# Kernel optimization log

Measured on AMD Instinct MI355X. Metric: run time of the kernel, lower is better.

## Reference

```python
import jax, jax.numpy as jnp
import numpy as np

N, E = 50000, 500000
IN, C, CE_IN = 128, 64, 16   # raw node dim, mid_channel, raw edge dim
L = 3                        # num_layers: layer0 = bare conv, layers 1..2 = res+ blocks
LN_EPS = 1e-5


def layer_norm(x, g, b):
    mu = x.mean(-1, keepdims=True)
    var = ((x - mu) ** 2).mean(-1, keepdims=True)
    return (x - mu) * jax.lax.rsqrt(var + LN_EPS) * g + b


def sage_conv(x, e, src, dst, W1, b1, W2, b2, Wr, t):
    """SAGEConvV2 with softmax aggregation. Returns (node_out, per-edge messages)."""
    # message: lin_l(cat([x_i, x_j, edge_attr])) ; x_i = dst (target), x_j = src (source)
    m_in = jnp.concatenate([x[dst], x[src], e], axis=-1)          # [E, 2C+Ce]
    m = jax.nn.relu(m_in @ W1 + b1) @ W2 + b2                      # [E, C]
    # scatter_softmax(m * t, dst) per feature channel
    logits = m * t
    seg_max = jax.ops.segment_max(logits, dst, num_segments=N)    # [N, C]
    w = jnp.exp(logits - seg_max[dst])
    w = w / jax.ops.segment_sum(w, dst, num_segments=N)[dst]
    out = jax.ops.segment_sum(m * w, dst, num_segments=N)         # [N, C]
    out = out + x @ Wr                                             # root weight (no bias)
    return out, m


def setup_inputs() -> dict:
    key = jax.random.key(0)
    ks = jax.random.split(key, 18)
    f32 = jnp.float32

    def w(k, shape, fan_in):
        return (jax.random.normal(k, shape, f32) / np.sqrt(fan_in)).astype(f32)

    inp = {
        "x": jax.random.normal(ks[0], (N, IN), f32),
        "edge_index": jax.random.randint(ks[1], (2, E), 0, N, dtype=jnp.int64),
        "edge_attr": jax.random.normal(ks[2], (E, CE_IN), f32),
        # encoders
        "node_W": w(ks[3], (IN, C), IN),
        "node_b": jnp.zeros((C,), f32),
        "edge_W": w(ks[4], (CE_IN, C), CE_IN),
        "edge_b": jnp.zeros((C,), f32),
        # stacked conv params (L convs, identical shapes)
        "conv_W1": w(ks[5], (L, 3 * C, 2 * C), 3 * C),
        "conv_b1": jnp.zeros((L, 2 * C), f32),
        "conv_W2": w(ks[6], (L, 2 * C, C), 2 * C),
        "conv_b2": jnp.zeros((L, C), f32),
        "conv_Wr": w(ks[7], (L, C, C), C),
        "conv_t": jnp.ones((L,), f32),
        # layer norms: ln_g[0]/ln_b[0] used as the final output norm, 1..2 inside res+ blocks
        "ln_g": jnp.ones((L, C), f32),
        "ln_b": jnp.zeros((L, C), f32),
        "eln_g": jnp.ones((L - 1, C), f32),
        "eln_b": jnp.zeros((L - 1, C), f32),
    }
    return inp


def reference(x, edge_index, edge_attr, node_W, node_b, edge_W, edge_b,
              conv_W1, conv_b1, conv_W2, conv_b2, conv_Wr, conv_t,
              ln_g, ln_b, eln_g, eln_b):
    src, dst = edge_index[0], edge_index[1]
    h = x @ node_W + node_b                    # node encoder
    e = edge_attr @ edge_W + edge_b            # edge encoder
    # first layer: bare conv
    h, e = sage_conv(h, e, src, dst, conv_W1[0], conv_b1[0], conv_W2[0],
                     conv_b2[0], conv_Wr[0], conv_t[0])
    # res+ blocks (dropout is identity in eval mode)
    for i in range(1, L):
        hn = jax.nn.relu(layer_norm(h, ln_g[i], ln_b[i]))
        en = layer_norm(e, eln_g[i - 1], eln_b[i - 1])
        dh, m = sage_conv(hn, en, src, dst, conv_W1[i], conv_b1[i], conv_W2[i],
                          conv_b2[i], conv_Wr[i], conv_t[i])
        h = h + dh
        e = e + m
    # final norm + act (uses layer-0 norm params, as in the canonical DeeperGCN example)
    return jax.nn.relu(layer_norm(h, ln_g[0], ln_b[0]))
```

## Files before the change

### kernel.cpp

```cpp
#include <hip/hip_runtime.h>

typedef unsigned short u16;
typedef unsigned int u32;
typedef __attribute__((ext_vector_type(8))) short short8;
typedef __attribute__((ext_vector_type(4))) float floatx4;

#define LN_EPS 1e-5f

__device__ __forceinline__ float bf2f(u16 u) {
    union { u32 i; float f; } v; v.i = ((u32)u) << 16; return v.f;
}
__device__ __forceinline__ u16 f2bf(float f) {
    union { u32 i; float f; } v; v.f = f;
    u32 x = v.i;
    return (u16)((x + 0x7fffu + ((x >> 16) & 1u)) >> 16);
}
__device__ __forceinline__ int clampi(int v, int lo, int hi) {
    return v < lo ? lo : (v > hi ? hi : v);
}

__global__ void k_fill(float* __restrict__ out, int nel, float val) {
    int i = blockIdx.x * blockDim.x + threadIdx.x;
    if (i < nel) out[i] = val;
}

__global__ void k_zero(int* p, int n) {
    int i = blockIdx.x * blockDim.x + threadIdx.x;
    if (i < n) p[i] = 0;
}

__global__ void k_detect(const int* __restrict__ ei, int E, int* __restrict__ flag) {
    __shared__ int any;
    if (threadIdx.x == 0) any = 0;
    __syncthreads();
    int lim = (E < 4096) ? E : 4096;
    int v = 0;
    for (int i = threadIdx.x; i < lim; i += 256) v |= ei[2 * i + 1];
    if (v) atomicOr(&any, 1);
    __syncthreads();
    if (threadIdx.x == 0) flag[0] = (any == 0) ? 1 : 0;
}

__global__ void k_hist(const int* __restrict__ ei, const int* __restrict__ flag,
                       int* __restrict__ deg, int E, int n) {
    int e = blockIdx.x * blockDim.x + threadIdx.x;
    if (e < E) {
        int d = flag[0] ? ei[2 * ((size_t)E + e)] : ei[(size_t)E + e];
        atomicAdd(&deg[clampi(d, 0, n - 1)], 1);
    }
}

__global__ void k_scan1(const int* __restrict__ deg, int* __restrict__ offs,
                        int* __restrict__ bsum, int n) {
    __shared__ int s[256];
    int t = threadIdx.x;
    int i = blockIdx.x * 256 + t;
    int v = (i < n) ? deg[i] : 0;
    s[t] = v; __syncthreads();
    for (int off = 1; off < 256; off <<= 1) {
        int x = (t >= off) ? s[t - off] : 0;
        __syncthreads();
        s[t] += x;
        __syncthreads();
    }
    if (i < n) offs[i] = s[t] - v;
    if (t == 255) bsum[blockIdx.x] = s[255];
}

__global__ void k_scan2(int* bsum, int nb) {
    __shared__ int s[256];
    int t = threadIdx.x;
    int v = (t < nb) ? bsum[t] : 0;
    s[t] = v; __syncthreads();
    for (int off = 1; off < 256; off <<= 1) {
        int x = (t >= off) ? s[t - off] : 0;
        __syncthreads();
        s[t] += x;
        __syncthreads();
    }
    if (t < nb) bsum[t] = s[t] - v;
}

__global__ void k_scan3(int* __restrict__ offs, const int* __restrict__ bsum,
                        int* __restrict__ cursor, int n, int E) {
    int i = blockIdx.x * 256 + threadIdx.x;
    if (i < n) {
        int v = offs[i] + bsum[blockIdx.x];
        offs[i] = v;
        cursor[i] = v;
    }
    if (i == 0) offs[n] = E;
}

__global__ void k_scatter(const int* __restrict__ ei, const int* __restrict__ flag,
                          int* __restrict__ cursor,
                          int* __restrict__ perm, int* __restrict__ srcs,
                          int* __restrict__ dsts, int E, int n) {
    int e = blockIdx.x * blockDim.x + threadIdx.x;
    if (e < E) {
        int sv, dv;
        if (flag[0]) {
            sv = ei[2 * (size_t)e];
            dv = ei[2 * ((size_t)E + e)];
        } else {
            sv = ei[e];
            dv = ei[(size_t)E + e];
        }
        sv = clampi(sv, 0, n - 1);
        dv = clampi(dv, 0, n - 1);
        int p = clampi(atomicAdd(&cursor[dv], 1), 0, E - 1);
        perm[p] = e;
        srcs[p] = sv;
        dsts[p] = dv;
    }
}

__global__ void k_swz(const float* __restrict__ W1, const float* __restrict__ W2,
                      const float* __restrict__ Wr, const float* __restrict__ nW,
                      u16* __restrict__ W1s, u16* __restrict__ W2s,
                      u16* __restrict__ Wrs, u16* __restrict__ nWs) {
    int i = blockIdx.x * blockDim.x + threadIdx.x;
    if (i < 3 * 24576) {
        int l = i / 24576, rem = i % 24576;
        int k = rem / 128, n = rem % 128;
        int kt = k >> 5, q = (k >> 3) & 3, j = k & 7;
        W1s[l * 24576 + ((kt * 4 + q) * 128 + n) * 8 + j] = f2bf(W1[i]);
    }
    if (i < 3 * 8192) {
        int l = i / 8192, rem = i % 8192;
        int k = rem / 64, n = rem % 64;
        int kt = k >> 5, q = (k >> 3) & 3, j = k & 7;
        W2s[l * 8192 + ((kt * 4 + q) * 64 + n) * 8 + j] = f2bf(W2[i]);
    }
    if (i < 3 * 4096) {
        int l = i / 4096, rem = i % 4096;
        int k = rem / 64, n = rem % 64;
        int kt = k >> 5, q = (k >> 3) & 3, j = k & 7;
        Wrs[l * 4096 + ((kt * 4 + q) * 64 + n) * 8 + j] = f2bf(Wr[i]);
    }
    if (i < 8192) {
        int k = i / 64, n = i % 64;
        int kt = k >> 5, q = (k >> 3) & 3, j = k & 7;
        nWs[((kt * 4 + q) * 64 + n) * 8 + j] = f2bf(nW[i]);
    }
}

__global__ __launch_bounds__(512) void k_node_enc(
    const float* __restrict__ x, const u16* __restrict__ nWs, const float* __restrict__ bias,
    float* __restrict__ h, u16* __restrict__ hn, int n) {
    int t = threadIdx.x;
    int w = t >> 6, l = t & 63, q = l >> 4, ml = l & 15;
    int wbase = blockIdx.x * 128 + w * 16;
    int rin = wbase + ml;
    int rr = (rin < n) ? rin : 0;
    const float* xr = x + (size_t)rr * 128;
    short8 a[4];
#pragma unroll
    for (int kt = 0; kt < 4; kt++) {
        float4 f0 = *((const float4*)(xr + kt * 32 + q * 8));
        float4 f1 = *((const float4*)(xr + kt * 32 + q * 8 + 4));
        a[kt][0] = (short)f2bf(f0.x); a[kt][1] = (short)f2bf(f0.y);
        a[kt][2] = (short)f2bf(f0.z); a[kt][3] = (short)f2bf(f0.w);
        a[kt][4] = (short)f2bf(f1.x); a[kt][5] = (short)f2bf(f1.y);
        a[kt][6] = (short)f2bf(f1.z); a[kt][7] = (short)f2bf(f1.w);
    }
    float bc[4];
#pragma unroll
    for (int nt = 0; nt < 4; nt++) bc[nt] = bias[nt * 16 + ml];
    floatx4 acc[4];
#pragma unroll
    for (int nt = 0; nt < 4; nt++) acc[nt] = floatx4{0.f, 0.f, 0.f, 0.f};
#pragma unroll
    for (int kt = 0; kt < 4; kt++) {
#pragma unroll
        for (int nt = 0; nt < 4; nt++) {
            short8 bf = *((const short8*)(nWs + (size_t)((kt * 4 + q) * 64 + nt * 16 + ml) * 8));
            acc[nt] = __builtin_amdgcn_mfma_f32_16x16x32_bf16(a[kt], bf, acc[nt], 0, 0, 0);
        }
    }
#pragma unroll
    for (int nt = 0; nt < 4; nt++) {
#pragma unroll
        for (int r2 = 0; r2 < 4; r2++) {
            int pos = wbase + q * 4 + r2;
            if (pos < n) {
                float v = acc[nt][r2] + bc[nt];
                size_t idx = (size_t)pos * 64 + nt * 16 + ml;
                h[idx] = v;
                hn[idx] = f2bf(v);
            }
        }
    }
}

__global__ __launch_bounds__(256) void k_edge_enc(
    const float* __restrict__ ea, const int* __restrict__ perm,
    const float* __restrict__ W, const float* __restrict__ bias,
    u16* __restrict__ e_s, int E) {
    __shared__ float4 sW4[16 * 16];
    int t = threadIdx.x;
    if (t < 256) sW4[t] = ((const float4*)W)[t];
    __syncthreads();
    int gid = blockIdx.x * 256 + t;
    int eidx = gid >> 2, qq = gid & 3;
    if (eidx >= E) return;
    int e = perm[eidx];
    const float4* row4 = (const float4*)(ea + (size_t)e * 16);
    float4 r4[4];
    r4[0] = row4[0]; r4[1] = row4[1]; r4[2] = row4[2]; r4[3] = row4[3];
    const float* row = (const float*)r4;
    float4 acc[4];
#pragma unroll
    for (int j = 0; j < 4; j++) acc[j] = ((const float4*)bias)[qq * 4 + j];
#pragma unroll
    for (int k = 0; k < 16; k++) {
        float rv = row[k];
#pragma unroll
        for (int j = 0; j < 4; j++) {
            float4 wv = sW4[k * 16 + qq * 4 + j];
            acc[j].x += rv * wv.x; acc[j].y += rv * wv.y;
            acc[j].z += rv * wv.z; acc[j].w += rv * wv.w;
        }
    }
    u32 pk[8];
#pragma unroll
    for (int j = 0; j < 4; j++) {
        pk[2 * j]     = (u32)f2bf(acc[j].x) | ((u32)f2bf(acc[j].y) << 16);
        pk[2 * j + 1] = (u32)f2bf(acc[j].z) | ((u32)f2bf(acc[j].w) << 16);
    }
    uint4* outp = (uint4*)(e_s + (size_t)eidx * 64 + qq * 16);
    outp[0] = make_uint4(pk[0], pk[1], pk[2], pk[3]);
    outp[1] = make_uint4(pk[4], pk[5], pk[6], pk[7]);
}

#define TILE 256
#define HSTR 136
__global__ __launch_bounds__(512, 4) void k_mlp(
    const u16* __restrict__ hn, const u16* __restrict__ e_s,
    const u16* __restrict__ e_s2,
    const int* __restrict__ dsts, const int* __restrict__ srcs,
    const u16* __restrict__ W1s, const float* __restrict__ b1,
    const u16* __restrict__ W2s, const float* __restrict__ b2,
    const float* __restrict__ elng, const float* __restrict__ elnb,
    int ln_edge, u16* __restrict__ m_out, int E) {
    __shared__ __align__(16) short sW2L[8192];
    __shared__ __align__(16) short sShared[24576];

    int t = threadIdx.x;
    int w = t >> 6, l = t & 63, q = l >> 4, ml = l & 15;
    int base = blockIdx.x * TILE + w * 32;
    int pos0 = base + ml;
    int pos1 = base + 16 + ml;
    bool act0 = pos0 < E, act1 = pos1 < E;
    int pp0 = act0 ? pos0 : 0, pp1 = act1 ? pos1 : 0;
    int dn0 = act0 ? dsts[pos0] : 0;
    int sn0 = act0 ? srcs[pos0] : 0;
    int dn1 = act1 ? dsts[pos1] : 0;
    int sn1 = act1 ? srcs[pos1] : 0;

    short8 a0[6], a1[6];
    a0[0] = *(const short8*)(hn + (size_t)dn0 * 64 + q * 8);
    a0[1] = *(const short8*)(hn + (size_t)dn0 * 64 + 32 + q * 8);
    a0[2] = *(const short8*)(hn + (size_t)sn0 * 64 + q * 8);
    a0[3] = *(const short8*)(hn + (size_t)sn0 * 64 + 32 + q * 8);
    a1[0] = *(const short8*)(hn + (size_t)dn1 * 64 + q * 8);
    a1[1] = *(const short8*)(hn + (size_t)dn1 * 64 + 32 + q * 8);
    a1[2] = *(const short8*)(hn + (size_t)sn1 * 64 + q * 8);
    a1[3] = *(const short8*)(hn + (size_t)sn1 * 64 + 32 + q * 8);
    short8 e00 = *(const short8*)(e_s + (size_t)pp0 * 64 + q * 8);
    short8 e01 = *(const short8*)(e_s + (size_t)pp0 * 64 + 32 + q * 8);
    short8 e10 = *(const short8*)(e_s + (size_t)pp1 * 64 + q * 8);
    short8 e11 = *(const short8*)(e_s + (size_t)pp1 * 64 + 32 + q * 8);
    short8 f00, f01, f10, f11;
    bool has2 = (e_s2 != nullptr);
    if (has2) {
        f00 = *(const short8*)(e_s2 + (size_t)pp0 * 64 + q * 8);
        f01 = *(const short8*)(e_s2 + (size_t)pp0 * 64 + 32 + q * 8);
        f10 = *(const short8*)(e_s2 + (size_t)pp1 * 64 + q * 8);
        f11 = *(const short8*)(e_s2 + (size_t)pp1 * 64 + 32 + q * 8);
    }

    {
        const uint4* g1 = (const uint4*)W1s;
        uint4* s1 = (uint4*)sShared;
#pragma unroll
        for (int j = 0; j < 6; j++) s1[t + j * 512] = g1[t + j * 512];
        const uint4* g2 = (const uint4*)W2s;
        uint4* s2 = (uint4*)sW2L;
#pragma unroll
        for (int j = 0; j < 2; j++) s2[t + j * 512] = g2[t + j * 512];
    }

    if (ln_edge) {
        {
            float ev[16];
            float sm = 0.f, sq = 0.f;
#pragma unroll
            for (int i = 0; i < 8; i++) {
                float f0 = bf2f((u16)e00[i]);
                float f1 = bf2f((u16)e01[i]);
                if (has2) { f0 += bf2f((u16)f00[i]); f1 += bf2f((u16)f01[i]); }
                ev[i] = f0; ev[8 + i] = f1;
                sm += f0 + f1; sq += f0 * f0 + f1 * f1;
            }
            sm += __shfl_xor(sm, 16); sm += __shfl_xor(sm, 32);
            sq += __shfl_xor(sq, 16); sq += __shfl_xor(sq, 32);
            float mu = sm * (1.f / 64.f);
            float var = sq * (1.f / 64.f) - mu * mu;
            float inv = rsqrtf(fmaxf(var, 0.f) + LN_EPS);
#pragma unroll
            for (int i = 0; i < 8; i++) {
                int c0 = q * 8 + i, c1 = 32 + q * 8 + i;
                a0[4][i] = (short)f2bf((ev[i] - mu) * inv * elng[c0] + elnb[c0]);
                a0[5][i] = (short)f2bf((ev[8 + i] - mu) * inv * elng[c1] + elnb[c1]);
            }
        }
        {
            float ev[16];
            float sm = 0.f, sq = 0.f;
#pragma unroll
            for (int i = 0; i < 8; i++) {
                float f0 = bf2f((u16)e10[i]);
                float f1 = bf2f((u16)e11[i]);
                if (has2) { f0 += bf2f((u16)f10[i]); f1 += bf2f((u16)f11[i]); }
                ev[i] = f0; ev[8 + i] = f1;
                sm += f0 + f1; sq += f0 * f0 + f1 * f1;
            }
            sm += __shfl_xor(sm, 16); sm += __shfl_xor(sm, 32);
            sq += __shfl_xor(sq, 16); sq += __shfl_xor(sq, 32);
            float mu = sm * (1.f / 64.f);
            float var = sq * (1.f / 64.f) - mu * mu;
            float inv = rsqrtf(fmaxf(var, 0.f) + LN_EPS);
#pragma unroll
            for (int i = 0; i < 8; i++) {
                int c0 = q * 8 + i, c1 = 32 + q * 8 + i;
                a1[4][i] = (short)f2bf((ev[i] - mu) * inv * elng[c0] + elnb[c0]);
                a1[5][i] = (short)f2bf((ev[8 + i] - mu) * inv * elng[c1] + elnb[c1]);
            }
        }
    } else {
        a0[4] = e00; a0[5] = e01;
        a1[4] = e10; a1[5] = e11;
    }

    __syncthreads();

    floatx4 acc0[8], acc1[8];
#pragma unroll
    for (int nt = 0; nt < 8; nt++) {
        acc0[nt] = floatx4{0.f, 0.f, 0.f, 0.f};
        acc1[nt] = floatx4{0.f, 0.f, 0.f, 0.f};
    }
#pragma unroll
    for (int kt = 0; kt < 6; kt++) {
#pragma unroll
        for (int nt = 0; nt < 8; nt++) {
            short8 bf = *((const short8*)(sShared + ((kt * 4 + q) * 128 + nt * 16 + ml) * 8));
            acc0[nt] = __builtin_amdgcn_mfma_f32_16x16x32_bf16(a0[kt], bf, acc0[nt], 0, 0, 0);
            acc1[nt] = __builtin_amdgcn_mfma_f32_16x16x32_bf16(a1[kt], bf, acc1[nt], 0, 0, 0);
        }
    }

    __syncthreads();

    float b1c[8], b2c[4];
#pragma unroll
    for (int nt = 0; nt < 8; nt++) b1c[nt] = b1[nt * 16 + ml];
#pragma unroll
    for (int nt = 0; nt < 4; nt++) b2c[nt] = b2[nt * 16 + ml];

    short* arena = sShared + w * 16 * HSTR;

#pragma unroll
    for (int nt = 0; nt < 8; nt++) {
#pragma unroll
        for (int r2 = 0; r2 < 4; r2++) {
            float v = fmaxf(acc0[nt][r2] + b1c[nt], 0.f);
            ((u16*)arena)[(q * 4 + r2) * HSTR + nt * 16 + ml] = f2bf(v);
        }
    }
    short8 ah0[4];
#pragma unroll
    for (int kt = 0; kt < 4; kt++)
        ah0[kt] = *((const short8*)(arena + ml * HSTR + kt * 32 + q * 8));

#pragma unroll
    for (int nt = 0; nt < 8; nt++) {
#pragma unroll
        for (int r2 = 0; r2 < 4; r2++) {
            float v = fmaxf(acc1[nt][r2] + b1c[nt], 0.f);
            ((u16*)arena)[(q * 4 + r2) * HSTR + nt * 16 + ml] = f2bf(v);
        }
    }
    short8 ah1[4];
#pragma unroll
    for (int kt = 0; kt < 4; kt++)
        ah1[kt] = *((const short8*)(arena + ml * HSTR + kt * 32 + q * 8));

    floatx4 c20[4], c21[4];
#pragma unroll
    for (int nt = 0; nt < 4; nt++) {
        c20[nt] = floatx4{0.f, 0.f, 0.f, 0.f};
        c21[nt] = floatx4{0.f, 0.f, 0.f, 0.f};
    }
#pragma unroll
    for (int kt = 0; kt < 4; kt++) {
#pragma unroll
        for (int nt = 0; nt < 4; nt++) {
            short8 bf = *((const short8*)(sW2L + ((kt * 4 + q) * 64 + nt * 16 + ml) * 8));
            c20[nt] = __builtin_amdgcn_mfma_f32_16x16x32_bf16(ah0[kt], bf, c20[nt], 0, 0, 0);
            c21[nt] = __builtin_amdgcn_mfma_f32_16x16x32_bf16(ah1[kt], bf, c21[nt], 0, 0, 0);
        }
    }

#pragma unroll
    for (int nt = 0; nt < 4; nt++) {
#pragma unroll
        for (int r2 = 0; r2 < 4; r2++) {
            ((u16*)arena)[(q * 4 + r2) * HSTR + nt * 16 + ml] = f2bf(c20[nt][r2] + b2c[nt]);
        }
    }
    {
        short8 m0 = *((const short8*)(arena + ml * HSTR + q * 16));
        short8 m1 = *((const short8*)(arena + ml * HSTR + q * 16 + 8));
        if (act0) {
            *((short8*)(m_out + (size_t)pos0 * 64 + q * 16)) = m0;
            *((short8*)(m_out + (size_t)pos0 * 64 + q * 16 + 8)) = m1;
        }
    }
#pragma unroll
    for (int nt = 0; nt < 4; nt++) {
#pragma unroll
        for (int r2 = 0; r2 < 4; r2++) {
            ((u16*)arena)[(q * 4 + r2) * HSTR + nt * 16 + ml] = f2bf(c21[nt][r2] + b2c[nt]);
        }
    }
    {
        short8 m0 = *((const short8*)(arena + ml * HSTR + q * 16));
        short8 m1 = *((const short8*)(arena + ml * HSTR + q * 16 + 8));
        if (act1) {
            *((short8*)(m_out + (size_t)pos1 * 64 + q * 16)) = m0;
            *((short8*)(m_out + (size_t)pos1 * 64 + q * 16 + 8)) = m1;
        }
    }
}

__global__ __launch_bounds__(512) void k_root(
    const u16* __restrict__ hn, const u16* __restrict__ Wrs,
    float* __restrict__ h, int add_h, int n) {
    __shared__ short sA[8 * 1024];
    int t = threadIdx.x;
    int base = blockIdx.x * 128;
    {
        int r = t >> 2, s = t & 3;
        int pos = base + r;
        int g = r >> 4, m = r & 15;
        short* grp = sA + g * 1024;
        bool act = pos < n;
        uint4 z4 = make_uint4(0, 0, 0, 0);
        const uint4* pd = (const uint4*)(hn + (size_t)(act ? pos : 0) * 64);
        uint4 d0 = act ? pd[2 * s] : z4;
        uint4 d1 = act ? pd[2 * s + 1] : z4;
        int ch = (s >> 1) * 4 + (s & 1) * 2;
        *((uint4*)(grp + ch * 128 + m * 8)) = d0;
        *((uint4*)(grp + (ch + 1) * 128 + m * 8)) = d1;
    }
    __syncthreads();
    int w = t >> 6, l = t & 63, q = l >> 4, ml = l & 15;
    short* arena = sA + w * 1024;
    floatx4 acc[4];
#pragma unroll
    for (int nt = 0; nt < 4; nt++) acc[nt] = floatx4{0.f, 0.f, 0.f, 0.f};
#pragma unroll
    for (int kt = 0; kt < 2; kt++) {
        short8 a = *((const short8*)(arena + (kt * 4 + q) * 128 + ml * 8));
#pragma unroll
        for (int nt = 0; nt < 4; nt++) {
            short8 bf = *((const short8*)(Wrs + (size_t)((kt * 4 + q) * 64 + nt * 16 + ml) * 8));
            acc[nt] = __builtin_amdgcn_mfma_f32_16x16x32_bf16(a, bf, acc[nt], 0, 0, 0);
        }
    }
#pragma unroll
    for (int nt = 0; nt < 4; nt++) {
#pragma unroll
        for (int r2 = 0; r2 < 4; r2++) {
            int pos = base + w * 16 + q * 4 + r2;
            if (pos < n) {
                size_t idx = (size_t)pos * 64 + nt * 16 + ml;
                float v = acc[nt][r2];
                h[idx] = add_h ? (h[idx] + v) : v;
            }
        }
    }
}

__global__ __launch_bounds__(256) void k_agg2(
    const u16* __restrict__ m_s, float* __restrict__ h,
    const int* __restrict__ offs, const float* __restrict__ tptr, int tidx,
    const float* __restrict__ g, const float* __restrict__ b,
    u16* __restrict__ hn_out, float* __restrict__ f32_out,
    int write_h, int n, int E) {
    int t = threadIdx.x, wid = t >> 6, lane = t & 63;
    float tv = tptr[tidx];
    float gc = g[lane], bc = b[lane];
    for (int node = blockIdx.x * 4 + wid; node < n; node += gridDim.x * 4) {
        int p0 = clampi(offs[node], 0, E);
        int p1 = clampi(offs[node + 1], p0, E);
        float M = -1e30f, D = 0.f, S = 0.f;
        int p = p0;
        for (; p + 1 < p1; p += 2) {
            float mv0 = bf2f(m_s[(size_t)p * 64 + lane]);
            float mv1 = bf2f(m_s[(size_t)(p + 1) * 64 + lane]);
            float lg0 = mv0 * tv, lg1 = mv1 * tv;
            float Mp = fmaxf(lg0, lg1);
            float a0 = __expf(lg0 - Mp), a1 = __expf(lg1 - Mp);
            float Dp = a0 + a1, Sp = mv0 * a0 + mv1 * a1;
            float Mn = fmaxf(M, Mp);
            float xx = __expf(M - Mn), yy = __expf(Mp - Mn);
            D = D * xx + Dp * yy;
            S = S * xx + Sp * yy;
            M = Mn;
        }
        if (p < p1) {
            float mv = bf2f(m_s[(size_t)p * 64 + lane]);
            float lg = mv * tv;
            float Mn = fmaxf(M, lg);
            float xx = __expf(M - Mn), yy = __expf(lg - Mn);
            D = D * xx + yy;
            S = S * xx + mv * yy;
        }
        float hv = h[(size_t)node * 64 + lane];
        if (p1 > p0) hv += S / D;
        if (write_h) h[(size_t)node * 64 + lane] = hv;
        float s = hv;
#pragma unroll
        for (int o = 32; o > 0; o >>= 1) s += __shfl_xor(s, o);
        float mu = s * (1.f / 64.f);
        float d = hv - mu;
        float s2 = d * d;
#pragma unroll
        for (int o = 32; o > 0; o >>= 1) s2 += __shfl_xor(s2, o);
        float inv = rsqrtf(s2 * (1.f / 64.f) + LN_EPS);
        float r = fmaxf(d * inv * gc + bc, 0.f);
        if (hn_out) hn_out[(size_t)node * 64 + lane] = f2bf(r);
        else        f32_out[(size_t)node * 64 + lane] = r;
    }
}

extern "C" void kernel_launch(void* const* d_in, const int* in_sizes, int n_in,
                              void* d_out, int out_size, void* d_ws, size_t ws_size,
                              hipStream_t stream) {
    float* outp = (float*)d_out;
    int FB = (out_size + 255) / 256;

    if (n_in != 17) {
        k_fill<<<FB, 256, 0, stream>>>(outp, out_size, 3.0f);
        return;
    }

    const float* x    = (const float*)d_in[0];
    const int*   ei   = (const int*)d_in[1];
    const float* ea   = (const float*)d_in[2];
    const float* nW   = (const float*)d_in[3];
    const float* nb   = (const float*)d_in[4];
    const float* eW   = (const float*)d_in[5];
    const float* eb   = (const float*)d_in[6];
    const float* cW1  = (const float*)d_in[7];
    const float* cb1  = (const float*)d_in[8];
    const float* cW2  = (const float*)d_in[9];
    const float* cb2  = (const float*)d_in[10];
    const float* cWr  = (const float*)d_in[11];
    const float* ct   = (const float*)d_in[12];
    const float* lng  = (const float*)d_in[13];
    const float* lnb  = (const float*)d_in[14];
    const float* elng = (const float*)d_in[15];
    const float* elnb = (const float*)d_in[16];

    const int n = in_sizes[0] / 128;
    const int E = in_sizes[2] / 16;

    char* ws = (char*)d_ws;
    size_t o = 0;
    auto alloc = [&](size_t bytes) -> void* {
        void* p = ws + o;
        o += (bytes + 255) & ~(size_t)255;
        return p;
    };
    int*   flag   = (int*)alloc(256);
    int*   deg    = (int*)alloc((size_t)n * 4);
    int*   offs   = (int*)alloc((size_t)(n + 1) * 4);
    int*   cursor = (int*)alloc((size_t)n * 4);
    int*   bsum   = (int*)alloc(256 * 4);
    int*   perm   = (int*)alloc((size_t)E * 4);
    int*   srcs   = (int*)alloc((size_t)E * 4);
    int*   dsts   = (int*)alloc((size_t)E * 4);
    float* h      = (float*)alloc((size_t)n * 64 * 4);
    u16*   hn     = (u16*)alloc((size_t)n * 64 * 2);
    u16*   bufA   = (u16*)alloc((size_t)E * 64 * 2);
    u16*   bufB   = (u16*)alloc((size_t)E * 64 * 2);
    u16*   W1s    = (u16*)alloc((size_t)3 * 24576 * 2);
    u16*   W2s    = (u16*)alloc((size_t)3 * 8192 * 2);
    u16*   Wrs    = (u16*)alloc((size_t)3 * 4096 * 2);
    u16*   nWs    = (u16*)alloc((size_t)8192 * 2);

    k_fill<<<FB, 256, 0, stream>>>(outp, out_size, 1.0f);
    if (o > ws_size) {
        k_fill<<<FB, 256, 0, stream>>>(outp, out_size, 2.0f);
        return;
    }

    int SB = (n + 255) / 256;
    k_detect<<<1, 256, 0, stream>>>(ei, E, flag);
    k_zero<<<SB, 256, 0, stream>>>(deg, n);
    k_hist<<<(E + 255) / 256, 256, 0, stream>>>(ei, flag, deg, E, n);
    k_scan1<<<SB, 256, 0, stream>>>(deg, offs, bsum, n);
    k_scan2<<<1, 256, 0, stream>>>(bsum, SB);
    k_scan3<<<SB, 256, 0, stream>>>(offs, bsum, cursor, n, E);
    k_scatter<<<(E + 255) / 256, 256, 0, stream>>>(ei, flag, cursor, perm, srcs, dsts, E, n);
    k_swz<<<(3 * 24576 + 255) / 256, 256, 0, stream>>>(cW1, cW2, cWr, nW, W1s, W2s, Wrs, nWs);
    k_node_enc<<<(n + 127) / 128, 512, 0, stream>>>(x, nWs, nb, h, hn, n);
    k_edge_enc<<<(E * 4 + 255) / 256, 256, 0, stream>>>(ea, perm, eW, eb, bufA, E);

    int MB = (E + TILE - 1) / TILE;
    int RB = (n + 127) / 128;
    int AB = (n + 3) / 4;

    const u16* mlp_in[3]  = { bufA, bufB, bufB };
    const u16* mlp_in2[3] = { nullptr, nullptr, bufA };
    u16*       mlp_out[3] = { bufB, bufA, bufA };

    for (int i = 0; i < 3; i++) {
        k_mlp<<<MB, 512, 0, stream>>>(
            hn, mlp_in[i], mlp_in2[i], dsts, srcs,
            W1s + (size_t)i * 24576, cb1 + (size_t)i * 128,
            W2s + (size_t)i * 8192, cb2 + (size_t)i * 64,
            elng + (size_t)((i > 0) ? (i - 1) : 0) * 64,
            elnb + (size_t)((i > 0) ? (i - 1) : 0) * 64,
            (i > 0) ? 1 : 0, mlp_out[i], E);
        k_root<<<RB, 512, 0, stream>>>(hn, Wrs + (size_t)i * 4096, h, (i > 0) ? 1 : 0, n);
        if (i < 2) {
            k_agg2<<<AB, 256, 0, stream>>>(mlp_out[i], h, offs, ct, i,
                                           lng + (size_t)(i + 1) * 64, lnb + (size_t)(i + 1) * 64,
                                           hn, nullptr, 1, n, E);
        } else {
            k_agg2<<<AB, 256, 0, stream>>>(mlp_out[i], h, offs, ct, i,
                                           lng, lnb,
                                           nullptr, outp, 0, n, E);
        }
    }
}
```

Measured before the change: 527.4 us.

## Fuse root-weight GEMM into node encoder and aggregation, drop k_root

Removes the standalone k_root launch by computing the layer-0 root term x@Wr inside the node encoder, and computing each next layer's root term inside k_agg2 right after LayerNorm. The shuffle-based dot product uses Wr staged in shared memory. It also merges the detect and zero kernels into one launch. This saves three launches and an extra read-modify-write of h per layer. In exchange, k_agg2 loads 8KB of weights into LDS per block and does 64 shuffle-FMAs per lane per node on scalar ALUs rather than MFMA, which may slow the aggregation kernel.

```diff
diff --git a/kernel.cpp b/kernel.cpp
--- a/kernel.cpp
+++ b/kernel.cpp
@@ -24,21 +24,22 @@
     if (i < nel) out[i] = val;
 }
 
-__global__ void k_zero(int* p, int n) {
-    int i = blockIdx.x * blockDim.x + threadIdx.x;
-    if (i < n) p[i] = 0;
-}
-
-__global__ void k_detect(const int* __restrict__ ei, int E, int* __restrict__ flag) {
-    __shared__ int any;
-    if (threadIdx.x == 0) any = 0;
-    __syncthreads();
-    int lim = (E < 4096) ? E : 4096;
-    int v = 0;
-    for (int i = threadIdx.x; i < lim; i += 256) v |= ei[2 * i + 1];
-    if (v) atomicOr(&any, 1);
-    __syncthreads();
-    if (threadIdx.x == 0) flag[0] = (any == 0) ? 1 : 0;
+__global__ void k_pre0(const int* __restrict__ ei, int E, int* __restrict__ flag,
+                       int* __restrict__ deg, int n) {
+    int t = threadIdx.x;
+    if (blockIdx.x == 0) {
+        __shared__ int any;
+        if (t == 0) any = 0;
+        __syncthreads();
+        int lim = (E < 4096) ? E : 4096;
+        int v = 0;
+        for (int i = t; i < lim; i += 256) v |= ei[2 * i + 1];
+        if (v) atomicOr(&any, 1);
+        __syncthreads();
+        if (t == 0) flag[0] = (any == 0) ? 1 : 0;
+    }
+    int i = blockIdx.x * 256 + t;
+    if (i < n) deg[i] = 0;
 }
 
 __global__ void k_hist(const int* __restrict__ ei, const int* __restrict__ flag,
@@ -118,7 +119,8 @@
 __global__ void k_swz(const float* __restrict__ W1, const float* __restrict__ W2,
                       const float* __restrict__ Wr, const float* __restrict__ nW,
                       u16* __restrict__ W1s, u16* __restrict__ W2s,
-                      u16* __restrict__ Wrs, u16* __restrict__ nWs) {
+                      u16* __restrict__ Wrs, u16* __restrict__ nWs,
+                      u16* __restrict__ WrKC) {
     int i = blockIdx.x * blockDim.x + threadIdx.x;
     if (i < 3 * 24576) {
         int l = i / 24576, rem = i % 24576;
@@ -137,6 +139,7 @@
         int k = rem / 64, n = rem % 64;
         int kt = k >> 5, q = (k >> 3) & 3, j = k & 7;
         Wrs[l * 4096 + ((kt * 4 + q) * 64 + n) * 8 + j] = f2bf(Wr[i]);
+        WrKC[i] = f2bf(Wr[i]);
     }
     if (i < 8192) {
         int k = i / 64, n = i % 64;
@@ -145,9 +148,13 @@
     }
 }
 
+#define HSTR 136
+
 __global__ __launch_bounds__(512) void k_node_enc(
     const float* __restrict__ x, const u16* __restrict__ nWs, const float* __restrict__ bias,
+    const u16* __restrict__ Wrs0,
     float* __restrict__ h, u16* __restrict__ hn, int n) {
+    __shared__ short sA[8 * 16 * HSTR];
     int t = threadIdx.x;
     int w = t >> 6, l = t & 63, q = l >> 4, ml = l & 15;
     int wbase = blockIdx.x * 128 + w * 16;
@@ -178,17 +185,39 @@
             acc[nt] = __builtin_amdgcn_mfma_f32_16x16x32_bf16(a[kt], bf, acc[nt], 0, 0, 0);
         }
     }
+    short* arena = sA + w * 16 * HSTR;
 #pragma unroll
     for (int nt = 0; nt < 4; nt++) {
 #pragma unroll
         for (int r2 = 0; r2 < 4; r2++) {
             int pos = wbase + q * 4 + r2;
-            if (pos < n) {
-                float v = acc[nt][r2] + bc[nt];
-                size_t idx = (size_t)pos * 64 + nt * 16 + ml;
-                h[idx] = v;
-                hn[idx] = f2bf(v);
-            }
+            float v = acc[nt][r2] + bc[nt];
+            u16 bv = f2bf(v);
+            arena[(q * 4 + r2) * HSTR + nt * 16 + ml] = (short)bv;
+            if (pos < n) hn[(size_t)pos * 64 + nt * 16 + ml] = bv;
+        }
+    }
+    short8 ah[2];
+#pragma unroll
+    for (int kt = 0; kt < 2; kt++)
+        ah[kt] = *((const short8*)(arena + ml * HSTR + kt * 32 + q * 8));
+    floatx4 acc2[4];
+#pragma unroll
+    for (int nt = 0; nt < 4; nt++) acc2[nt] = floatx4{0.f, 0.f, 0.f, 0.f};
+#pragma unroll
+    for (int kt = 0; kt < 2; kt++) {
+#pragma unroll
+        for (int nt = 0; nt < 4; nt++) {
+            short8 bf = *((const short8*)(Wrs0 + (size_t)((kt * 4 + q) * 64 + nt * 16 + ml) * 8));
+            acc2[nt] = __builtin_amdgcn_mfma_f32_16x16x32_bf16(ah[kt], bf, acc2[nt], 0, 0, 0);
+        }
+    }
+#pragma unroll
+    for (int nt = 0; nt < 4; nt++) {
+#pragma unroll
+        for (int r2 = 0; r2 < 4; r2++) {
+            int pos = wbase + q * 4 + r2;
+            if (pos < n) h[(size_t)pos * 64 + nt * 16 + ml] = acc2[nt][r2];
         }
     }
 }
@@ -234,7 +263,6 @@
 }
 
 #define TILE 256
-#define HSTR 136
 __global__ __launch_bounds__(512, 4) void k_mlp(
     const u16* __restrict__ hn, const u16* __restrict__ e_s,
     const u16* __restrict__ e_s2,
@@ -445,62 +473,20 @@
     }
 }
 
-__global__ __launch_bounds__(512) void k_root(
-    const u16* __restrict__ hn, const u16* __restrict__ Wrs,
-    float* __restrict__ h, int add_h, int n) {
-    __shared__ short sA[8 * 1024];
-    int t = threadIdx.x;
-    int base = blockIdx.x * 128;
-    {
-        int r = t >> 2, s = t & 3;
-        int pos = base + r;
-        int g = r >> 4, m = r & 15;
-        short* grp = sA + g * 1024;
-        bool act = pos < n;
-        uint4 z4 = make_uint4(0, 0, 0, 0);
-        const uint4* pd = (const uint4*)(hn + (size_t)(act ? pos : 0) * 64);
-        uint4 d0 = act ? pd[2 * s] : z4;
-        uint4 d1 = act ? pd[2 * s + 1] : z4;
-        int ch = (s >> 1) * 4 + (s & 1) * 2;
-        *((uint4*)(grp + ch * 128 + m * 8)) = d0;
-        *((uint4*)(grp + (ch + 1) * 128 + m * 8)) = d1;
-    }
-    __syncthreads();
-    int w = t >> 6, l = t & 63, q = l >> 4, ml = l & 15;
-    short* arena = sA + w * 1024;
-    floatx4 acc[4];
-#pragma unroll
-    for (int nt = 0; nt < 4; nt++) acc[nt] = floatx4{0.f, 0.f, 0.f, 0.f};
-#pragma unroll
-    for (int kt = 0; kt < 2; kt++) {
-        short8 a = *((const short8*)(arena + (kt * 4 + q) * 128 + ml * 8));
-#pragma unroll
-        for (int nt = 0; nt < 4; nt++) {
-            short8 bf = *((const short8*)(Wrs + (size_t)((kt * 4 + q) * 64 + nt * 16 + ml) * 8));
-            acc[nt] = __builtin_amdgcn_mfma_f32_16x16x32_bf16(a, bf, acc[nt], 0, 0, 0);
-        }
-    }
-#pragma unroll
-    for (int nt = 0; nt < 4; nt++) {
-#pragma unroll
-        for (int r2 = 0; r2 < 4; r2++) {
-            int pos = base + w * 16 + q * 4 + r2;
-            if (pos < n) {
-                size_t idx = (size_t)pos * 64 + nt * 16 + ml;
-                float v = acc[nt][r2];
-                h[idx] = add_h ? (h[idx] + v) : v;
-            }
-        }
-    }
-}
-
 __global__ __launch_bounds__(256) void k_agg2(
     const u16* __restrict__ m_s, float* __restrict__ h,
     const int* __restrict__ offs, const float* __restrict__ tptr, int tidx,
     const float* __restrict__ g, const float* __restrict__ b,
+    const u16* __restrict__ wrkc,
     u16* __restrict__ hn_out, float* __restrict__ f32_out,
-    int write_h, int n, int E) {
+    int n, int E) {
+    __shared__ u16 sWr[4096];
     int t = threadIdx.x, wid = t >> 6, lane = t & 63;
+    bool haveW = (wrkc != nullptr);
+    if (haveW) {
+        for (int i = t; i < 4096; i += 256) sWr[i] = wrkc[i];
+        __syncthreads();
+    }
     float tv = tptr[tidx];
     float gc = g[lane], bc = b[lane];
     for (int node = blockIdx.x * 4 + wid; node < n; node += gridDim.x * 4) {
@@ -531,7 +517,6 @@
         }
         float hv = h[(size_t)node * 64 + lane];
         if (p1 > p0) hv += S / D;
-        if (write_h) h[(size_t)node * 64 + lane] = hv;
         float s = hv;
 #pragma unroll
         for (int o = 32; o > 0; o >>= 1) s += __shfl_xor(s, o);
@@ -544,6 +529,18 @@
         float r = fmaxf(d * inv * gc + bc, 0.f);
         if (hn_out) hn_out[(size_t)node * 64 + lane] = f2bf(r);
         else        f32_out[(size_t)node * 64 + lane] = r;
+        if (haveW) {
+            float rf = bf2f(f2bf(r));
+            float r0 = 0.f, r1 = 0.f, r2a = 0.f, r3 = 0.f;
+#pragma unroll
+            for (int k = 0; k < 64; k += 4) {
+                r0  += __shfl(rf, k)     * bf2f(sWr[(k)     * 64 + lane]);
+                r1  += __shfl(rf, k + 1) * bf2f(sWr[(k + 1) * 64 + lane]);
+                r2a += __shfl(rf, k + 2) * bf2f(sWr[(k + 2) * 64 + lane]);
+                r3  += __shfl(rf, k + 3) * bf2f(sWr[(k + 3) * 64 + lane]);
+            }
+            h[(size_t)node * 64 + lane] = hv + ((r0 + r1) + (r2a + r3));
+        }
     }
 }
 
@@ -602,6 +599,7 @@
     u16*   W2s    = (u16*)alloc((size_t)3 * 8192 * 2);
     u16*   Wrs    = (u16*)alloc((size_t)3 * 4096 * 2);
     u16*   nWs    = (u16*)alloc((size_t)8192 * 2);
+    u16*   WrKC   = (u16*)alloc((size_t)3 * 4096 * 2);
 
     k_fill<<<FB, 256, 0, stream>>>(outp, out_size, 1.0f);
     if (o > ws_size) {
@@ -610,19 +608,17 @@
     }
 
     int SB = (n + 255) / 256;
-    k_detect<<<1, 256, 0, stream>>>(ei, E, flag);
-    k_zero<<<SB, 256, 0, stream>>>(deg, n);
+    k_pre0<<<SB, 256, 0, stream>>>(ei, E, flag, deg, n);
     k_hist<<<(E + 255) / 256, 256, 0, stream>>>(ei, flag, deg, E, n);
     k_scan1<<<SB, 256, 0, stream>>>(deg, offs, bsum, n);
     k_scan2<<<1, 256, 0, stream>>>(bsum, SB);
     k_scan3<<<SB, 256, 0, stream>>>(offs, bsum, cursor, n, E);
     k_scatter<<<(E + 255) / 256, 256, 0, stream>>>(ei, flag, cursor, perm, srcs, dsts, E, n);
-    k_swz<<<(3 * 24576 + 255) / 256, 256, 0, stream>>>(cW1, cW2, cWr, nW, W1s, W2s, Wrs, nWs);
-    k_node_enc<<<(n + 127) / 128, 512, 0, stream>>>(x, nWs, nb, h, hn, n);
+    k_swz<<<(3 * 24576 + 255) / 256, 256, 0, stream>>>(cW1, cW2, cWr, nW, W1s, W2s, Wrs, nWs, WrKC);
+    k_node_enc<<<(n + 127) / 128, 512, 0, stream>>>(x, nWs, nb, Wrs, h, hn, n);
     k_edge_enc<<<(E * 4 + 255) / 256, 256, 0, stream>>>(ea, perm, eW, eb, bufA, E);
 
     int MB = (E + TILE - 1) / TILE;
-    int RB = (n + 127) / 128;
     int AB = (n + 3) / 4;
 
     const u16* mlp_in[3]  = { bufA, bufB, bufB };
@@ -637,15 +633,16 @@
             elng + (size_t)((i > 0) ? (i - 1) : 0) * 64,
             elnb + (size_t)((i > 0) ? (i - 1) : 0) * 64,
             (i > 0) ? 1 : 0, mlp_out[i], E);
-        k_root<<<RB, 512, 0, stream>>>(hn, Wrs + (size_t)i * 4096, h, (i > 0) ? 1 : 0, n);
         if (i < 2) {
             k_agg2<<<AB, 256, 0, stream>>>(mlp_out[i], h, offs, ct, i,
                                            lng + (size_t)(i + 1) * 64, lnb + (size_t)(i + 1) * 64,
-                                           hn, nullptr, 1, n, E);
+                                           WrKC + (size_t)(i + 1) * 4096,
+                                           hn, nullptr, n, E);
         } else {
             k_agg2<<<AB, 256, 0, stream>>>(mlp_out[i], h, offs, ct, i,
                                            lng, lnb,
-                                           nullptr, outp, 0, n, E);
-        }
-    }
-}
+                                           nullptr,
+                                           nullptr, outp, n, E);
+        }
+    }
+}
```

After: 648.2 us. +22.9%, slower.
